# Performance work log

Hardware: AMD Instinct MI355X
Metric: run time of the kernel (lower is better)

## Reference

```python
import jax, jax.numpy as jnp
import numpy as np

N_EXPERTS = 16
TOP_K = 2
D_MODEL = 1024
D_FF = 1024
D_FF_SHARED = 2048
T_TOKENS = 4096


def setup_inputs() -> dict:
    key = jax.random.key(0)
    ks = jax.random.split(key, 7)
    s = 0.02
    return {
        "hidden_states": jax.random.normal(ks[0], (T_TOKENS, D_MODEL), jnp.float32),
        "gate_weight": jax.random.normal(ks[1], (N_EXPERTS, D_MODEL), jnp.float32) * s,
        "expert_gate_up": jax.random.normal(ks[2], (N_EXPERTS, 2 * D_FF, D_MODEL), jnp.float32) * s,
        "expert_down": jax.random.normal(ks[3], (N_EXPERTS, D_MODEL, D_FF), jnp.float32) * s,
        "shared_gate_up": jax.random.normal(ks[4], (2 * D_FF_SHARED, D_MODEL), jnp.float32) * s,
        "shared_down": jax.random.normal(ks[5], (D_MODEL, D_FF_SHARED), jnp.float32) * s,
        "shared_expert_gate_weight": jax.random.normal(ks[6], (1, D_MODEL), jnp.float32) * s,
    }


def _moe_forward(x, gate_weight, expert_gate_up, expert_down):
    T = x.shape[0]
    E = gate_weight.shape[0]
    # Router: top-k over logits, softmax over the selected logits (fp32)
    router_logits = x @ gate_weight.T                      # [T, E]
    topk_logits, topk_ids = jax.lax.top_k(router_logits, TOP_K)
    topk_weights = jax.nn.softmax(topk_logits.astype(jnp.float32), axis=-1)
    # Dense combine matrix C[t, e] = routing weight of expert e for token t
    combine = jnp.zeros((T, E), jnp.float32).at[
        jnp.arange(T)[:, None], topk_ids
    ].add(topk_weights)                                    # [T, E]

    # Scan over experts to avoid materializing [E, T, d]
    def body(acc, inputs):
        w_gu, w_d, c_e = inputs                            # [2F,d], [d,F], [T]
        gu = x @ w_gu.T                                    # [T, 2F]
        g, u = gu[:, :D_FF], gu[:, D_FF:]
        h = jax.nn.silu(g) * u                             # [T, F]
        acc = acc + c_e[:, None] * (h @ w_d.T)             # [T, d]
        return acc, None

    acc0 = jnp.zeros_like(x)
    moe_out, _ = jax.lax.scan(body, acc0, (expert_gate_up, expert_down, combine.T))
    return moe_out


def _shared_expert(x, shared_gate_up, shared_down, shared_expert_gate_weight):
    gu = x @ shared_gate_up.T                              # [T, 2Fs]
    mid = gu.shape[-1] // 2
    h = jax.nn.silu(gu[:, :mid]) * gu[:, mid:]
    out = h @ shared_down.T                                # [T, d]
    gate = jax.nn.sigmoid(x @ shared_expert_gate_weight.T)  # [T, 1]
    return out * gate


def reference(hidden_states, gate_weight, expert_gate_up, expert_down,
              shared_gate_up, shared_down, shared_expert_gate_weight):
    moe_out = _moe_forward(hidden_states, gate_weight, expert_gate_up, expert_down)
    shared_out = _shared_expert(hidden_states, shared_gate_up, shared_down,
                                shared_expert_gate_weight)
    return moe_out + shared_out
```

## Files before the change

kernel.cpp:

```cpp
#include <hip/hip_runtime.h>
#include <hip/hip_bf16.h>

#define T_TOKENS 4096
#define D_MODEL  1024
#define N_EXP    16
#define D_FF     1024
#define D_FF_SH  2048
#define MAX_T256 48

typedef __attribute__((ext_vector_type(8))) short short8;
typedef __attribute__((ext_vector_type(4))) float float4v;

__device__ __forceinline__ short f2bf(float f) {
    union { float f; unsigned u; } c; c.f = f;
    unsigned u = c.u + 0x7fffu + ((c.u >> 16) & 1u);
    return (short)(u >> 16);
}

__device__ __forceinline__ void gload16(const void* g, void* l) {
    __builtin_amdgcn_global_load_lds(
        (const __attribute__((address_space(1))) void*)g,
        (__attribute__((address_space(3))) void*)l, 16, 0, 0);
}

__global__ __launch_bounds__(256) void convert_all_kernel(
    const float* __restrict__ s0, short* __restrict__ d0,
    const float* __restrict__ s1, short* __restrict__ d1,
    const float* __restrict__ s2, short* __restrict__ d2,
    const float* __restrict__ s3, short* __restrict__ d3) {
    int c = blockIdx.x * 256 + threadIdx.x;
    const float* s; short* d; int off;
    if      (c < 4194304) { s = s0; d = d0; off = c; }
    else if (c < 6291456) { s = s1; d = d1; off = c - 4194304; }
    else if (c < 6815744) { s = s2; d = d2; off = c - 6291456; }
    else                  { s = s3; d = d3; off = c - 6815744; }
    size_t i = (size_t)off * 8;
    float4 a = *(const float4*)(s + i);
    float4 b = *(const float4*)(s + i + 4);
    union { short sh[8]; int4 v; } p;
    p.sh[0] = f2bf(a.x); p.sh[1] = f2bf(a.y); p.sh[2] = f2bf(a.z); p.sh[3] = f2bf(a.w);
    p.sh[4] = f2bf(b.x); p.sh[5] = f2bf(b.y); p.sh[6] = f2bf(b.z); p.sh[7] = f2bf(b.w);
    *(int4*)(d + i) = p.v;
}

__global__ __launch_bounds__(256) void router_kernel(
    const float* __restrict__ x, const float* __restrict__ gw, const float* __restrict__ sgw,
    short* __restrict__ xb, int* __restrict__ topk_id, float* __restrict__ topk_w,
    float* __restrict__ gate, int* __restrict__ counts) {
    __shared__ float gwl[17 * 1024];
    int tid = threadIdx.x;
#pragma unroll
    for (int i = 0; i < 16; i++)
        *(float4*)&gwl[tid * 4 + i * 1024] = *(const float4*)&gw[tid * 4 + i * 1024];
    *(float4*)&gwl[16384 + tid * 4] = *(const float4*)&sgw[tid * 4];
    __syncthreads();

    int wave = tid >> 6, lane = tid & 63;
    int t0 = blockIdx.x * 16 + wave * 4;

    float acc[4][17];
#pragma unroll
    for (int tt = 0; tt < 4; tt++)
#pragma unroll
        for (int e = 0; e < 17; e++) acc[tt][e] = 0.f;

#pragma unroll
    for (int i = 0; i < 4; i++) {
        int d = lane * 4 + i * 256;
        float4 xv[4];
#pragma unroll
        for (int tt = 0; tt < 4; tt++) {
            xv[tt] = *(const float4*)&x[(size_t)(t0 + tt) * D_MODEL + d];
            union { short sh[4]; int2 v; } p;
            p.sh[0] = f2bf(xv[tt].x); p.sh[1] = f2bf(xv[tt].y);
            p.sh[2] = f2bf(xv[tt].z); p.sh[3] = f2bf(xv[tt].w);
            *(int2*)&xb[(size_t)(t0 + tt) * D_MODEL + d] = p.v;
        }
#pragma unroll
        for (int e = 0; e < 17; e++) {
            float4 g = *(const float4*)&gwl[e * 1024 + d];
#pragma unroll
            for (int tt = 0; tt < 4; tt++)
                acc[tt][e] += xv[tt].x * g.x + xv[tt].y * g.y + xv[tt].z * g.z + xv[tt].w * g.w;
        }
    }

#pragma unroll
    for (int tt = 0; tt < 4; tt++)
#pragma unroll
        for (int e = 0; e < 17; e++)
            for (int off = 32; off; off >>= 1) acc[tt][e] += __shfl_xor(acc[tt][e], off);

    if (lane == 0) {
#pragma unroll
        for (int tt = 0; tt < 4; tt++) {
            int t = t0 + tt;
            float v1 = -1e30f, v2 = -1e30f; int i1 = 0, i2 = 0;
#pragma unroll
            for (int e = 0; e < 16; e++) {
                float v = acc[tt][e];
                if (v > v1) { v2 = v1; i2 = i1; v1 = v; i1 = e; }
                else if (v > v2) { v2 = v; i2 = e; }
            }
            float e2 = expf(v2 - v1);
            float s = 1.f + e2;
            topk_id[t * 2] = i1; topk_id[t * 2 + 1] = i2;
            topk_w[t * 2] = 1.f / s; topk_w[t * 2 + 1] = e2 / s;
            gate[t] = 1.f / (1.f + expf(-acc[tt][16]));
            atomicAdd(&counts[i1], 1); atomicAdd(&counts[i2], 1);
        }
    }
}

__global__ void offsets_kernel(const int* __restrict__ counts, int* __restrict__ offsets,
                               int* __restrict__ cursor, int* __restrict__ tile_map,
                               int* __restrict__ n_tiles) {
    if (threadIdx.x == 0) {
        int off = 0, nt = 0;
        for (int e = 0; e < N_EXP; e++) {
            offsets[e] = off; cursor[e] = off;
            int c = counts[e];
            for (int r = 0; r < c; r += 256) tile_map[nt++] = (e << 16) | (r >> 8);
            off += c;
        }
        n_tiles[0] = nt;
    }
}

__global__ __launch_bounds__(256) void scatter_kernel(
    const int* __restrict__ topk_id, const float* __restrict__ topk_w,
    int* __restrict__ cursor, int* __restrict__ tok_list, float* __restrict__ tok_w,
    int* __restrict__ slot_of) {
    int t = blockIdx.x * 256 + threadIdx.x;
#pragma unroll
    for (int k = 0; k < 2; k++) {
        int e = topk_id[t * 2 + k];
        int pos = atomicAdd(&cursor[e], 1);
        tok_list[pos] = t;
        tok_w[pos] = topk_w[t * 2 + k];
        slot_of[t * 2 + k] = pos;
    }
}

__global__ __launch_bounds__(512, 2) void gemm1_kernel(
    const short* __restrict__ xb,
    const short* __restrict__ Wexp,
    const short* __restrict__ Wsh,
    short* __restrict__ Hexp,
    short* __restrict__ Hsh,
    const int* __restrict__ tok_list,
    const int* __restrict__ offsets, const int* __restrict__ counts,
    const int* __restrict__ tile_map, const int* __restrict__ n_tiles) {
    int bx = blockIdx.x, by = blockIdx.y;
    int count, row0, dff;
    const int* idx = nullptr;
    const short* Wg; short* Hout;
    if (bx < MAX_T256) {
        if (by >= 8 || bx >= n_tiles[0]) return;
        int tm = tile_map[bx];
        int e = tm >> 16; row0 = (tm & 0xffff) << 8;
        count = counts[e];
        int base = offsets[e];
        idx = tok_list + base;
        Wg = Wexp + (size_t)e * 2 * D_FF * D_MODEL;
        Hout = Hexp + (size_t)base * D_FF;
        dff = D_FF;
    } else {
        row0 = (bx - MAX_T256) * 256; count = T_TOKENS;
        Wg = Wsh; Hout = Hsh; dff = D_FF_SH;
    }
    int col0 = by * 128;
    const short* Wu = Wg + (size_t)dff * D_MODEL;

    __shared__ char lds[65536];

    int t = threadIdx.x;
    int wave = t >> 6, lane = t & 63;
    int wm = (wave & 3) * 64, wn = (wave >> 2) * 64;
    int fr = lane & 15, fk2 = (lane >> 4) * 16;

    float4v accg[4][4], accu[4][4];
#pragma unroll
    for (int i = 0; i < 4; i++)
#pragma unroll
        for (int j = 0; j < 4; j++) { accg[i][j] = (float4v)0.f; accu[i][j] = (float4v)0.f; }

    int rA = t >> 2;
    int cq = (t & 3) * 8;
    int r0c = min(row0 + rA, count - 1);
    int r1c = min(row0 + rA + 128, count - 1);
    int g0 = idx ? idx[r0c] : r0c;
    int g1 = idx ? idx[r1c] : r1c;
    const short* aP0 = xb + (size_t)g0 * D_MODEL + cq;
    const short* aP1 = xb + (size_t)g1 * D_MODEL + cq;
    const short* bgP = Wg + (size_t)(col0 + rA) * D_MODEL + cq;
    const short* buP = Wu + (size_t)(col0 + rA) * D_MODEL + cq;
    int lo = t * 16;

    gload16(aP0, lds + lo);
    gload16(aP1, lds + 8192 + lo);
    gload16(bgP, lds + 16384 + lo);
    gload16(buP, lds + 24576 + lo);

    const int NK = D_MODEL / 32;
    for (int k = 0; k < NK; k++) {
        __syncthreads();
        if (k + 1 < NK) {
            int s = ((k + 1) & 1) * 32768;
            int off = (k + 1) * 32;
            gload16(aP0 + off, lds + s + lo);
            gload16(aP1 + off, lds + s + 8192 + lo);
            gload16(bgP + off, lds + s + 16384 + lo);
            gload16(buP + off, lds + s + 24576 + lo);
        }
        int sb = (k & 1) * 32768;
        short8 af[4], bgf[4], buf[4];
#pragma unroll
        for (int i = 0; i < 4; i++)
            af[i] = *(const short8*)(lds + sb + (wm + i * 16 + fr) * 64 + fk2);
#pragma unroll
        for (int j = 0; j < 4; j++) {
            bgf[j] = *(const short8*)(lds + sb + 16384 + (wn + j * 16 + fr) * 64 + fk2);
            buf[j] = *(const short8*)(lds + sb + 24576 + (wn + j * 16 + fr) * 64 + fk2);
        }
#pragma unroll
        for (int i = 0; i < 4; i++)
#pragma unroll
            for (int j = 0; j < 4; j++) {
                accg[i][j] = __builtin_amdgcn_mfma_f32_16x16x32_bf16(af[i], bgf[j], accg[i][j], 0, 0, 0);
                accu[i][j] = __builtin_amdgcn_mfma_f32_16x16x32_bf16(af[i], buf[j], accu[i][j], 0, 0, 0);
            }
    }

    int erow = (lane >> 4) * 4;
    int ecol = lane & 15;
#pragma unroll
    for (int i = 0; i < 4; i++)
#pragma unroll
        for (int j = 0; j < 4; j++)
#pragma unroll
            for (int r = 0; r < 4; r++) {
                int row = wm + i * 16 + erow + r;
                if (row0 + row < count) {
                    float g = accg[i][j][r], u = accu[i][j][r];
                    float h = g / (1.f + expf(-g)) * u;
                    Hout[(size_t)(row0 + row) * dff + col0 + wn + j * 16 + ecol] = f2bf(h);
                }
            }
}

__global__ __launch_bounds__(512, 2) void gemm2_kernel(
    const short* __restrict__ Hexp, const short* __restrict__ Hsh,
    const short* __restrict__ Wdexp,
    const short* __restrict__ Wdsh,
    float* __restrict__ oslots,
    float* __restrict__ out,
    const float* __restrict__ tok_w, const float* __restrict__ gate,
    const int* __restrict__ offsets, const int* __restrict__ counts,
    const int* __restrict__ tile_map, const int* __restrict__ n_tiles) {
    int bx = blockIdx.x, by = blockIdx.y;
    int count, row0, K, base;
    const short* Ab; const short* B;
    bool shared_part;
    if (bx < MAX_T256) {
        if (bx >= n_tiles[0]) return;
        int tm = tile_map[bx];
        int e = tm >> 16; row0 = (tm & 0xffff) << 8;
        count = counts[e]; base = offsets[e];
        Ab = Hexp + (size_t)base * D_FF; K = D_FF;
        B = Wdexp + (size_t)e * D_MODEL * D_FF;
        shared_part = false;
    } else {
        row0 = (bx - MAX_T256) * 256; count = T_TOKENS; base = 0;
        Ab = Hsh; K = D_FF_SH; B = Wdsh; shared_part = true;
    }
    int col0 = by * 128;

    __shared__ char lds[49152];

    int t = threadIdx.x;
    int wave = t >> 6, lane = t & 63;
    int wm = (wave & 3) * 64, wn = (wave >> 2) * 64;
    int fr = lane & 15, fk2 = (lane >> 4) * 16;

    float4v acc[4][4];
#pragma unroll
    for (int i = 0; i < 4; i++)
#pragma unroll
        for (int j = 0; j < 4; j++) acc[i][j] = (float4v)0.f;

    int rA = t >> 2;
    int cq = (t & 3) * 8;
    int r0c = min(row0 + rA, count - 1);
    int r1c = min(row0 + rA + 128, count - 1);
    const short* aP0 = Ab + (size_t)r0c * K + cq;
    const short* aP1 = Ab + (size_t)r1c * K + cq;
    const short* bP  = B + (size_t)(col0 + rA) * K + cq;
    int lo = t * 16;

    gload16(aP0, lds + lo);
    gload16(aP1, lds + 8192 + lo);
    gload16(bP,  lds + 16384 + lo);

    const int NK = K / 32;
    for (int k = 0; k < NK; k++) {
        __syncthreads();
        if (k + 1 < NK) {
            int s = ((k + 1) & 1) * 24576;
            int off = (k + 1) * 32;
            gload16(aP0 + off, lds + s + lo);
            gload16(aP1 + off, lds + s + 8192 + lo);
            gload16(bP + off,  lds + s + 16384 + lo);
        }
        int sb = (k & 1) * 24576;
        short8 af[4], bf[4];
#pragma unroll
        for (int i = 0; i < 4; i++)
            af[i] = *(const short8*)(lds + sb + (wm + i * 16 + fr) * 64 + fk2);
#pragma unroll
        for (int j = 0; j < 4; j++)
            bf[j] = *(const short8*)(lds + sb + 16384 + (wn + j * 16 + fr) * 64 + fk2);
#pragma unroll
        for (int i = 0; i < 4; i++)
#pragma unroll
            for (int j = 0; j < 4; j++)
                acc[i][j] = __builtin_amdgcn_mfma_f32_16x16x32_bf16(af[i], bf[j], acc[i][j], 0, 0, 0);
    }

    int erow = (lane >> 4) * 4;
    int ecol = lane & 15;
#pragma unroll
    for (int i = 0; i < 4; i++)
#pragma unroll
        for (int j = 0; j < 4; j++)
#pragma unroll
            for (int r = 0; r < 4; r++) {
                int row = wm + i * 16 + erow + r;
                if (row0 + row < count) {
                    float v = acc[i][j][r];
                    int col = col0 + wn + j * 16 + ecol;
                    if (!shared_part) {
                        int slot = base + row0 + row;
                        oslots[(size_t)slot * D_MODEL + col] = tok_w[slot] * v;
                    } else {
                        out[(size_t)(row0 + row) * D_MODEL + col] = gate[row0 + row] * v;
                    }
                }
            }
}

__global__ __launch_bounds__(256) void combine_kernel(
    float* __restrict__ out, const float* __restrict__ oslots,
    const int* __restrict__ slot_of) {
    int t = blockIdx.x;
    int sA = slot_of[t * 2], sB = slot_of[t * 2 + 1];
    int d = threadIdx.x * 4;
    float4 o = *(float4*)&out[(size_t)t * D_MODEL + d];
    float4 a = *(const float4*)&oslots[(size_t)sA * D_MODEL + d];
    float4 b = *(const float4*)&oslots[(size_t)sB * D_MODEL + d];
    o.x += a.x + b.x; o.y += a.y + b.y; o.z += a.z + b.z; o.w += a.w + b.w;
    *(float4*)&out[(size_t)t * D_MODEL + d] = o;
}

extern "C" void kernel_launch(void* const* d_in, const int* in_sizes, int n_in,
                              void* d_out, int out_size, void* d_ws, size_t ws_size,
                              hipStream_t stream) {
    const float* x     = (const float*)d_in[0];
    const float* gw    = (const float*)d_in[1];
    const float* egu   = (const float*)d_in[2];
    const float* edown = (const float*)d_in[3];
    const float* sgu   = (const float*)d_in[4];
    const float* sdown = (const float*)d_in[5];
    const float* sgate = (const float*)d_in[6];
    float* out = (float*)d_out;
    char* ws = (char*)d_ws;

    const size_t XB_OFF     = 0;
    const size_t WGU_OFF    = XB_OFF     + (size_t)4096*1024*2;
    const size_t WDOWN_OFF  = WGU_OFF    + (size_t)16*2048*1024*2;
    const size_t WSGU_OFF   = WDOWN_OFF  + (size_t)16*1024*1024*2;
    const size_t WSDOWN_OFF = WSGU_OFF   + (size_t)4096*1024*2;
    const size_t HEXP_OFF   = WSDOWN_OFF + (size_t)1024*2048*2;
    const size_t HSH_OFF    = HEXP_OFF   + (size_t)8192*1024*2;
    const size_t OSLOT_OFF  = HSH_OFF    + (size_t)4096*2048*2;
    const size_t TID_OFF    = OSLOT_OFF  + (size_t)8192*1024*4;
    const size_t TW_OFF     = TID_OFF    + 4096*2*4;
    const size_t GATE_OFF   = TW_OFF     + 4096*2*4;
    const size_t TOKL_OFF   = GATE_OFF   + 4096*4;
    const size_t TOKW_OFF   = TOKL_OFF   + 8192*4;
    const size_t SLOT_OFF   = TOKW_OFF   + 8192*4;
    const size_t CNT_OFF    = SLOT_OFF   + 8192*4;
    const size_t OFFS_OFF   = CNT_OFF    + 256;
    const size_t CUR_OFF    = OFFS_OFF   + 256;
    const size_t TMAP_OFF   = CUR_OFF    + 256;
    const size_t NT_OFF     = TMAP_OFF   + 512;

    short* xb      = (short*)(ws + XB_OFF);
    short* wgu_b   = (short*)(ws + WGU_OFF);
    short* wdown_b = (short*)(ws + WDOWN_OFF);
    short* wsgu_b  = (short*)(ws + WSGU_OFF);
    short* wsdn_b  = (short*)(ws + WSDOWN_OFF);
    short* h_exp   = (short*)(ws + HEXP_OFF);
    short* h_sh    = (short*)(ws + HSH_OFF);
    float* oslots  = (float*)(ws + OSLOT_OFF);
    int*   topk_id = (int*)(ws + TID_OFF);
    float* topk_w  = (float*)(ws + TW_OFF);
    float* gate    = (float*)(ws + GATE_OFF);
    int*   tok_l   = (int*)(ws + TOKL_OFF);
    float* tok_w   = (float*)(ws + TOKW_OFF);
    int*   slot_of = (int*)(ws + SLOT_OFF);
    int*   counts  = (int*)(ws + CNT_OFF);
    int*   offsets = (int*)(ws + OFFS_OFF);
    int*   cursor  = (int*)(ws + CUR_OFF);
    int*   tmap    = (int*)(ws + TMAP_OFF);
    int*   ntiles  = (int*)(ws + NT_OFF);

    hipMemsetAsync(counts, 0, 64, stream);

    convert_all_kernel<<<27648, 256, 0, stream>>>(egu, wgu_b, edown, wdown_b,
                                                  sgu, wsgu_b, sdown, wsdn_b);
    router_kernel<<<256, 256, 0, stream>>>(x, gw, sgate, xb, topk_id, topk_w, gate, counts);
    offsets_kernel<<<1, 64, 0, stream>>>(counts, offsets, cursor, tmap, ntiles);
    scatter_kernel<<<T_TOKENS / 256, 256, 0, stream>>>(topk_id, topk_w, cursor, tok_l, tok_w, slot_of);

    gemm1_kernel<<<dim3(MAX_T256 + 16, 16), 512, 0, stream>>>(
        xb, wgu_b, wsgu_b, h_exp, h_sh, tok_l, offsets, counts, tmap, ntiles);

    gemm2_kernel<<<dim3(MAX_T256 + 16, 8), 512, 0, stream>>>(
        h_exp, h_sh, wdown_b, wsdn_b, oslots, out, tok_w, gate, offsets, counts, tmap, ntiles);

    combine_kernel<<<T_TOKENS, 256, 0, stream>>>(out, oslots, slot_of);
}
```

Measured before the change: 604.8 us.

## Convert grouped GEMM kernels to persistent grid-stride tile scheduling

Both GEMM kernels now run a fixed grid of 512 and 384 blocks that loop over a flat tile index, covering the expert tiles first and then the shared-expert tiles. This replaces the padded 2D grids in which many blocks exited early. The aim is to cut the launch and tail cost of empty blocks and to balance work across CUs. A barrier is added between tiles so the LDS buffers can be reused, and the prologue of each new tile is no longer overlapped with the previous one.

```diff
diff --git a/kernel.cpp b/kernel.cpp
--- a/kernel.cpp
+++ b/kernel.cpp
@@ -6,7 +6,6 @@
 #define N_EXP    16
 #define D_FF     1024
 #define D_FF_SH  2048
-#define MAX_T256 48
 
 typedef __attribute__((ext_vector_type(8))) short short8;
 typedef __attribute__((ext_vector_type(4))) float float4v;
@@ -151,102 +150,108 @@
     const int* __restrict__ tok_list,
     const int* __restrict__ offsets, const int* __restrict__ counts,
     const int* __restrict__ tile_map, const int* __restrict__ n_tiles) {
-    int bx = blockIdx.x, by = blockIdx.y;
-    int count, row0, dff;
-    const int* idx = nullptr;
-    const short* Wg; short* Hout;
-    if (bx < MAX_T256) {
-        if (by >= 8 || bx >= n_tiles[0]) return;
-        int tm = tile_map[bx];
-        int e = tm >> 16; row0 = (tm & 0xffff) << 8;
-        count = counts[e];
-        int base = offsets[e];
-        idx = tok_list + base;
-        Wg = Wexp + (size_t)e * 2 * D_FF * D_MODEL;
-        Hout = Hexp + (size_t)base * D_FF;
-        dff = D_FF;
-    } else {
-        row0 = (bx - MAX_T256) * 256; count = T_TOKENS;
-        Wg = Wsh; Hout = Hsh; dff = D_FF_SH;
-    }
-    int col0 = by * 128;
-    const short* Wu = Wg + (size_t)dff * D_MODEL;
-
     __shared__ char lds[65536];
+
+    int nt = n_tiles[0];
+    int total = nt * 8 + 256;
 
     int t = threadIdx.x;
     int wave = t >> 6, lane = t & 63;
     int wm = (wave & 3) * 64, wn = (wave >> 2) * 64;
     int fr = lane & 15, fk2 = (lane >> 4) * 16;
-
-    float4v accg[4][4], accu[4][4];
-#pragma unroll
-    for (int i = 0; i < 4; i++)
-#pragma unroll
-        for (int j = 0; j < 4; j++) { accg[i][j] = (float4v)0.f; accu[i][j] = (float4v)0.f; }
-
     int rA = t >> 2;
     int cq = (t & 3) * 8;
-    int r0c = min(row0 + rA, count - 1);
-    int r1c = min(row0 + rA + 128, count - 1);
-    int g0 = idx ? idx[r0c] : r0c;
-    int g1 = idx ? idx[r1c] : r1c;
-    const short* aP0 = xb + (size_t)g0 * D_MODEL + cq;
-    const short* aP1 = xb + (size_t)g1 * D_MODEL + cq;
-    const short* bgP = Wg + (size_t)(col0 + rA) * D_MODEL + cq;
-    const short* buP = Wu + (size_t)(col0 + rA) * D_MODEL + cq;
     int lo = t * 16;
-
-    gload16(aP0, lds + lo);
-    gload16(aP1, lds + 8192 + lo);
-    gload16(bgP, lds + 16384 + lo);
-    gload16(buP, lds + 24576 + lo);
-
-    const int NK = D_MODEL / 32;
-    for (int k = 0; k < NK; k++) {
-        __syncthreads();
-        if (k + 1 < NK) {
-            int s = ((k + 1) & 1) * 32768;
-            int off = (k + 1) * 32;
-            gload16(aP0 + off, lds + s + lo);
-            gload16(aP1 + off, lds + s + 8192 + lo);
-            gload16(bgP + off, lds + s + 16384 + lo);
-            gload16(buP + off, lds + s + 24576 + lo);
-        }
-        int sb = (k & 1) * 32768;
-        short8 af[4], bgf[4], buf[4];
-#pragma unroll
-        for (int i = 0; i < 4; i++)
-            af[i] = *(const short8*)(lds + sb + (wm + i * 16 + fr) * 64 + fk2);
-#pragma unroll
-        for (int j = 0; j < 4; j++) {
-            bgf[j] = *(const short8*)(lds + sb + 16384 + (wn + j * 16 + fr) * 64 + fk2);
-            buf[j] = *(const short8*)(lds + sb + 24576 + (wn + j * 16 + fr) * 64 + fk2);
-        }
-#pragma unroll
-        for (int i = 0; i < 4; i++)
-#pragma unroll
-            for (int j = 0; j < 4; j++) {
-                accg[i][j] = __builtin_amdgcn_mfma_f32_16x16x32_bf16(af[i], bgf[j], accg[i][j], 0, 0, 0);
-                accu[i][j] = __builtin_amdgcn_mfma_f32_16x16x32_bf16(af[i], buf[j], accu[i][j], 0, 0, 0);
-            }
-    }
-
     int erow = (lane >> 4) * 4;
     int ecol = lane & 15;
-#pragma unroll
-    for (int i = 0; i < 4; i++)
-#pragma unroll
-        for (int j = 0; j < 4; j++)
-#pragma unroll
-            for (int r = 0; r < 4; r++) {
-                int row = wm + i * 16 + erow + r;
-                if (row0 + row < count) {
-                    float g = accg[i][j][r], u = accu[i][j][r];
-                    float h = g / (1.f + expf(-g)) * u;
-                    Hout[(size_t)(row0 + row) * dff + col0 + wn + j * 16 + ecol] = f2bf(h);
+
+    for (int it = blockIdx.x; it < total; it += gridDim.x) {
+        int count, row0, col0, dff;
+        const int* idx = nullptr;
+        const short* Wg; short* Hout;
+        if (it < nt * 8) {
+            int tm = tile_map[it >> 3];
+            int e = tm >> 16; row0 = (tm & 0xffff) << 8;
+            col0 = (it & 7) * 128;
+            count = counts[e];
+            int base = offsets[e];
+            idx = tok_list + base;
+            Wg = Wexp + (size_t)e * 2 * D_FF * D_MODEL;
+            Hout = Hexp + (size_t)base * D_FF;
+            dff = D_FF;
+        } else {
+            int s = it - nt * 8;
+            row0 = (s >> 4) * 256; col0 = (s & 15) * 128;
+            count = T_TOKENS;
+            Wg = Wsh; Hout = Hsh; dff = D_FF_SH;
+        }
+        const short* Wu = Wg + (size_t)dff * D_MODEL;
+
+        float4v accg[4][4], accu[4][4];
+#pragma unroll
+        for (int i = 0; i < 4; i++)
+#pragma unroll
+            for (int j = 0; j < 4; j++) { accg[i][j] = (float4v)0.f; accu[i][j] = (float4v)0.f; }
+
+        int r0c = min(row0 + rA, count - 1);
+        int r1c = min(row0 + rA + 128, count - 1);
+        int g0 = idx ? idx[r0c] : r0c;
+        int g1 = idx ? idx[r1c] : r1c;
+        const short* aP0 = xb + (size_t)g0 * D_MODEL + cq;
+        const short* aP1 = xb + (size_t)g1 * D_MODEL + cq;
+        const short* bgP = Wg + (size_t)(col0 + rA) * D_MODEL + cq;
+        const short* buP = Wu + (size_t)(col0 + rA) * D_MODEL + cq;
+
+        __syncthreads();
+        gload16(aP0, lds + lo);
+        gload16(aP1, lds + 8192 + lo);
+        gload16(bgP, lds + 16384 + lo);
+        gload16(buP, lds + 24576 + lo);
+
+        const int NK = D_MODEL / 32;
+        for (int k = 0; k < NK; k++) {
+            __syncthreads();
+            if (k + 1 < NK) {
+                int s = ((k + 1) & 1) * 32768;
+                int off = (k + 1) * 32;
+                gload16(aP0 + off, lds + s + lo);
+                gload16(aP1 + off, lds + s + 8192 + lo);
+                gload16(bgP + off, lds + s + 16384 + lo);
+                gload16(buP + off, lds + s + 24576 + lo);
+            }
+            int sb = (k & 1) * 32768;
+            short8 af[4], bgf[4], buf[4];
+#pragma unroll
+            for (int i = 0; i < 4; i++)
+                af[i] = *(const short8*)(lds + sb + (wm + i * 16 + fr) * 64 + fk2);
+#pragma unroll
+            for (int j = 0; j < 4; j++) {
+                bgf[j] = *(const short8*)(lds + sb + 16384 + (wn + j * 16 + fr) * 64 + fk2);
+                buf[j] = *(const short8*)(lds + sb + 24576 + (wn + j * 16 + fr) * 64 + fk2);
+            }
+#pragma unroll
+            for (int i = 0; i < 4; i++)
+#pragma unroll
+                for (int j = 0; j < 4; j++) {
+                    accg[i][j] = __builtin_amdgcn_mfma_f32_16x16x32_bf16(af[i], bgf[j], accg[i][j], 0, 0, 0);
+                    accu[i][j] = __builtin_amdgcn_mfma_f32_16x16x32_bf16(af[i], buf[j], accu[i][j], 0, 0, 0);
                 }
-            }
+        }
+
+#pragma unroll
+        for (int i = 0; i < 4; i++)
+#pragma unroll
+            for (int j = 0; j < 4; j++)
+#pragma unroll
+                for (int r = 0; r < 4; r++) {
+                    int row = wm + i * 16 + erow + r;
+                    if (row0 + row < count) {
+                        float g = accg[i][j][r], u = accu[i][j][r];
+                        float h = g / (1.f + expf(-g)) * u;
+                        Hout[(size_t)(row0 + row) * dff + col0 + wn + j * 16 + ecol] = f2bf(h);
+                    }
+                }
+    }
 }
 
 __global__ __launch_bounds__(512, 2) void gemm2_kernel(
@@ -258,95 +263,101 @@
     const float* __restrict__ tok_w, const float* __restrict__ gate,
     const int* __restrict__ offsets, const int* __restrict__ counts,
     const int* __restrict__ tile_map, const int* __restrict__ n_tiles) {
-    int bx = blockIdx.x, by = blockIdx.y;
-    int count, row0, K, base;
-    const short* Ab; const short* B;
-    bool shared_part;
-    if (bx < MAX_T256) {
-        if (bx >= n_tiles[0]) return;
-        int tm = tile_map[bx];
-        int e = tm >> 16; row0 = (tm & 0xffff) << 8;
-        count = counts[e]; base = offsets[e];
-        Ab = Hexp + (size_t)base * D_FF; K = D_FF;
-        B = Wdexp + (size_t)e * D_MODEL * D_FF;
-        shared_part = false;
-    } else {
-        row0 = (bx - MAX_T256) * 256; count = T_TOKENS; base = 0;
-        Ab = Hsh; K = D_FF_SH; B = Wdsh; shared_part = true;
-    }
-    int col0 = by * 128;
-
     __shared__ char lds[49152];
+
+    int nt = n_tiles[0];
+    int total = nt * 8 + 128;
 
     int t = threadIdx.x;
     int wave = t >> 6, lane = t & 63;
     int wm = (wave & 3) * 64, wn = (wave >> 2) * 64;
     int fr = lane & 15, fk2 = (lane >> 4) * 16;
-
-    float4v acc[4][4];
-#pragma unroll
-    for (int i = 0; i < 4; i++)
-#pragma unroll
-        for (int j = 0; j < 4; j++) acc[i][j] = (float4v)0.f;
-
     int rA = t >> 2;
     int cq = (t & 3) * 8;
-    int r0c = min(row0 + rA, count - 1);
-    int r1c = min(row0 + rA + 128, count - 1);
-    const short* aP0 = Ab + (size_t)r0c * K + cq;
-    const short* aP1 = Ab + (size_t)r1c * K + cq;
-    const short* bP  = B + (size_t)(col0 + rA) * K + cq;
     int lo = t * 16;
-
-    gload16(aP0, lds + lo);
-    gload16(aP1, lds + 8192 + lo);
-    gload16(bP,  lds + 16384 + lo);
-
-    const int NK = K / 32;
-    for (int k = 0; k < NK; k++) {
-        __syncthreads();
-        if (k + 1 < NK) {
-            int s = ((k + 1) & 1) * 24576;
-            int off = (k + 1) * 32;
-            gload16(aP0 + off, lds + s + lo);
-            gload16(aP1 + off, lds + s + 8192 + lo);
-            gload16(bP + off,  lds + s + 16384 + lo);
-        }
-        int sb = (k & 1) * 24576;
-        short8 af[4], bf[4];
-#pragma unroll
-        for (int i = 0; i < 4; i++)
-            af[i] = *(const short8*)(lds + sb + (wm + i * 16 + fr) * 64 + fk2);
-#pragma unroll
-        for (int j = 0; j < 4; j++)
-            bf[j] = *(const short8*)(lds + sb + 16384 + (wn + j * 16 + fr) * 64 + fk2);
-#pragma unroll
-        for (int i = 0; i < 4; i++)
-#pragma unroll
-            for (int j = 0; j < 4; j++)
-                acc[i][j] = __builtin_amdgcn_mfma_f32_16x16x32_bf16(af[i], bf[j], acc[i][j], 0, 0, 0);
-    }
-
     int erow = (lane >> 4) * 4;
     int ecol = lane & 15;
-#pragma unroll
-    for (int i = 0; i < 4; i++)
-#pragma unroll
-        for (int j = 0; j < 4; j++)
-#pragma unroll
-            for (int r = 0; r < 4; r++) {
-                int row = wm + i * 16 + erow + r;
-                if (row0 + row < count) {
-                    float v = acc[i][j][r];
-                    int col = col0 + wn + j * 16 + ecol;
-                    if (!shared_part) {
-                        int slot = base + row0 + row;
-                        oslots[(size_t)slot * D_MODEL + col] = tok_w[slot] * v;
-                    } else {
-                        out[(size_t)(row0 + row) * D_MODEL + col] = gate[row0 + row] * v;
+
+    for (int it = blockIdx.x; it < total; it += gridDim.x) {
+        int count, row0, col0, K, base;
+        const short* Ab; const short* B;
+        bool shared_part;
+        if (it < nt * 8) {
+            int tm = tile_map[it >> 3];
+            int e = tm >> 16; row0 = (tm & 0xffff) << 8;
+            col0 = (it & 7) * 128;
+            count = counts[e]; base = offsets[e];
+            Ab = Hexp + (size_t)base * D_FF; K = D_FF;
+            B = Wdexp + (size_t)e * D_MODEL * D_FF;
+            shared_part = false;
+        } else {
+            int s = it - nt * 8;
+            row0 = (s >> 3) * 256; col0 = (s & 7) * 128;
+            count = T_TOKENS; base = 0;
+            Ab = Hsh; K = D_FF_SH; B = Wdsh; shared_part = true;
+        }
+
+        float4v acc[4][4];
+#pragma unroll
+        for (int i = 0; i < 4; i++)
+#pragma unroll
+            for (int j = 0; j < 4; j++) acc[i][j] = (float4v)0.f;
+
+        int r0c = min(row0 + rA, count - 1);
+        int r1c = min(row0 + rA + 128, count - 1);
+        const short* aP0 = Ab + (size_t)r0c * K + cq;
+        const short* aP1 = Ab + (size_t)r1c * K + cq;
+        const short* bP  = B + (size_t)(col0 + rA) * K + cq;
+
+        __syncthreads();
+        gload16(aP0, lds + lo);
+        gload16(aP1, lds + 8192 + lo);
+        gload16(bP,  lds + 16384 + lo);
+
+        const int NK = K / 32;
+        for (int k = 0; k < NK; k++) {
+            __syncthreads();
+            if (k + 1 < NK) {
+                int s = ((k + 1) & 1) * 24576;
+                int off = (k + 1) * 32;
+                gload16(aP0 + off, lds + s + lo);
+                gload16(aP1 + off, lds + s + 8192 + lo);
+                gload16(bP + off,  lds + s + 16384 + lo);
+            }
+            int sb = (k & 1) * 24576;
+            short8 af[4], bf[4];
+#pragma unroll
+            for (int i = 0; i < 4; i++)
+                af[i] = *(const short8*)(lds + sb + (wm + i * 16 + fr) * 64 + fk2);
+#pragma unroll
+            for (int j = 0; j < 4; j++)
+                bf[j] = *(const short8*)(lds + sb + 16384 + (wn + j * 16 + fr) * 64 + fk2);
+#pragma unroll
+            for (int i = 0; i < 4; i++)
+#pragma unroll
+                for (int j = 0; j < 4; j++)
+                    acc[i][j] = __builtin_amdgcn_mfma_f32_16x16x32_bf16(af[i], bf[j], acc[i][j], 0, 0, 0);
+        }
+
+#pragma unroll
+        for (int i = 0; i < 4; i++)
+#pragma unroll
+            for (int j = 0; j < 4; j++)
+#pragma unroll
+                for (int r = 0; r < 4; r++) {
+                    int row = wm + i * 16 + erow + r;
+                    if (row0 + row < count) {
+                        float v = acc[i][j][r];
+                        int col = col0 + wn + j * 16 + ecol;
+                        if (!shared_part) {
+                            int slot = base + row0 + row;
+                            oslots[(size_t)slot * D_MODEL + col] = tok_w[slot] * v;
+                        } else {
+                            out[(size_t)(row0 + row) * D_MODEL + col] = gate[row0 + row] * v;
+                        }
                     }
                 }
-            }
+    }
 }
 
 __global__ __launch_bounds__(256) void combine_kernel(
@@ -423,10 +434,10 @@
     offsets_kernel<<<1, 64, 0, stream>>>(counts, offsets, cursor, tmap, ntiles);
     scatter_kernel<<<T_TOKENS / 256, 256, 0, stream>>>(topk_id, topk_w, cursor, tok_l, tok_w, slot_of);
 
-    gemm1_kernel<<<dim3(MAX_T256 + 16, 16), 512, 0, stream>>>(
+    gemm1_kernel<<<512, 512, 0, stream>>>(
         xb, wgu_b, wsgu_b, h_exp, h_sh, tok_l, offsets, counts, tmap, ntiles);
 
-    gemm2_kernel<<<dim3(MAX_T256 + 16, 8), 512, 0, stream>>>(
+    gemm2_kernel<<<384, 512, 0, stream>>>(
         h_exp, h_sh, wdown_b, wsdn_b, oslots, out, tok_w, gate, offsets, counts, tmap, ntiles);
 
     combine_kernel<<<T_TOKENS, 256, 0, stream>>>(out, oslots, slot_of);
```

New measurement: 618.3 us. 2.2% more time.
